# Performance work log

Hardware: AMD Instinct MI355X
Metric: run time of the kernel (lower is better)

The kernel has to match this reference:

```python
import jax, jax.numpy as jnp
import numpy as np

BINS = 200
DEPTH_MIN = 1.0
DEPTH_MAX = 80.0
ALPHA = 2.0
EPS = 1e-6
LOSS_WEIGHT = 1.0  # module attribute set externally in the repo; default 1.0
DMIN_LOG = float(np.log10(DEPTH_MIN))
INTERVAL = float((np.log10(DEPTH_MAX) - DMIN_LOG) / BINS)


def depth_to_bins_in_log(depth, mask):
    # truncation toward zero matches torch .to(torch.int)
    bins = ((jnp.log10(jnp.abs(depth)) - DMIN_LOG) / INTERVAL).astype(jnp.int32)
    bins = jnp.where(depth <= DEPTH_MIN, 0, bins)
    bins = jnp.where(depth >= DEPTH_MAX, BINS - 1, bins)
    bins = jnp.where(bins == BINS, BINS - 1, bins)
    bins = jnp.where(~mask, BINS + 1, bins)  # invalid pixels -> out-of-range id
    return bins


def setup_inputs() -> dict:
    key = jax.random.key(0)
    k1, k2, k3 = jax.random.split(key, 3)
    B, H, W = 4, 256, 384
    target = jax.random.uniform(k1, (B, 1, H, W), dtype=jnp.float32) * 100.0
    mask = jax.random.uniform(k2, (B, 1, H, W)) > 0.1
    pred_logit = jax.random.normal(k3, (B, BINS, H, W), dtype=jnp.float32)
    idx = jnp.arange(BINS, dtype=jnp.float32)
    # bins_weight[j, i] = exp(-alpha * (i - j)^2)
    bins_weight = jnp.exp(-ALPHA * (idx[None, :] - idx[:, None]) ** 2).astype(jnp.float32)
    return {"target": target, "mask": mask, "pred_logit": pred_logit, "bins_weight": bins_weight}


def reference(target, mask, pred_logit, bins_weight):
    B, C = pred_logit.shape[0], pred_logit.shape[1]
    gt_bins = depth_to_bins_in_log(target, mask)                 # [B,1,H,W] int32
    log_pred = jax.nn.log_softmax(pred_logit, axis=1)            # [B,C,H,W]
    log_pred = log_pred.reshape(B, C, -1).transpose(0, 2, 1)      # [B,N,C]
    gt_flat = gt_bins.reshape(B, -1)                              # [B,N]
    valid = gt_flat < C                                           # invalid rows -> zero weight
    # one_hot @ bins_weight is exactly a row-gather from bins_weight (zero row if invalid)
    weight = jnp.where(valid[..., None],
                       bins_weight[jnp.clip(gt_flat, 0, C - 1)],
                       jnp.zeros((), log_pred.dtype))             # [B,N,C]
    loss_pixels = -jnp.sum(weight * log_pred, axis=2)             # [B,N]
    valid_pixels = jnp.sum(mask).astype(log_pred.dtype)
    loss = jnp.sum(loss_pixels) / (valid_pixels + EPS)
    return loss * LOSS_WEIGHT
```

## Files before the change

kernel.cpp:

```cpp
#include <hip/hip_runtime.h>
#include <math.h>

#define C_BINS 200
#define PX 4

typedef float fv4 __attribute__((ext_vector_type(4)));
typedef int   iv4 __attribute__((ext_vector_type(4)));

__global__ __launch_bounds__(128) void dce_main_kernel(
    const float* __restrict__ target,
    const int*   __restrict__ mask,
    const float* __restrict__ logit,
    float*       __restrict__ ws,
    int HW)
{
    const int t  = blockIdx.x * blockDim.x + threadIdx.x;
    const int p0 = t * PX;
    const int b  = p0 / HW;
    const int hw = p0 - b * HW;

    const fv4 dep4 = *reinterpret_cast<const fv4*>(target + p0);
    const iv4 mk4  = *reinterpret_cast<const iv4*>(mask + p0);

    float gf[PX], valid[PX];
    #pragma unroll
    for (int j = 0; j < PX; ++j) {
        const float dj = dep4[j];
        int g;
        if (dj <= 1.0f) {
            g = 0;
        } else if (dj >= 80.0f) {
            g = 199;
        } else {
            g = (int)(log10f(dj) / 0.0095154499349597175f);
            g = (g > 199) ? 199 : g;
            g = (g < 0) ? 0 : g;
        }
        gf[j]    = (float)g;
        valid[j] = mk4[j] ? 1.0f : 0.0f;
    }

    const float* base = logit + (size_t)b * C_BINS * HW + hw;

    float m[PX], s[PX], dot[PX], sw[PX];
    #pragma unroll
    for (int j = 0; j < PX; ++j) { m[j] = -INFINITY; s[j] = 0.0f; dot[j] = 0.0f; sw[j] = 0.0f; }

    #pragma unroll 4
    for (int c = 0; c < C_BINS; ++c) {
        const fv4 x4 = __builtin_nontemporal_load(
            reinterpret_cast<const fv4*>(base + (size_t)c * HW));
        const float cf = (float)c;
        #pragma unroll
        for (int j = 0; j < PX; ++j) {
            const float x = x4[j];
            const float nm = fmaxf(m[j], x);
            const float e  = __expf(fminf(m[j], x) - nm);
            const bool  xg = x > m[j];
            s[j] = fmaf(s[j], xg ? e : 1.0f, xg ? 1.0f : e);
            m[j] = nm;
            const float d = cf - gf[j];
            const float w = __expf(-2.0f * d * d);
            dot[j] = fmaf(w, x, dot[j]);
            sw[j] += w;
        }
    }

    float lossp = 0.0f, vsum = 0.0f;
    #pragma unroll
    for (int j = 0; j < PX; ++j) {
        const float lse = m[j] + logf(s[j]);
        lossp += valid[j] * fmaf(lse, sw[j], -dot[j]);
        vsum  += valid[j];
    }

    #pragma unroll
    for (int off = 32; off > 0; off >>= 1) {
        lossp += __shfl_down(lossp, off);
        vsum  += __shfl_down(vsum, off);
    }
    __shared__ float sl[2], sv[2];
    const int wid = threadIdx.x >> 6;
    if ((threadIdx.x & 63) == 0) { sl[wid] = lossp; sv[wid] = vsum; }
    __syncthreads();
    if (threadIdx.x == 0) {
        atomicAdd(&ws[0], sl[0] + sl[1]);
        atomicAdd(&ws[1], sv[0] + sv[1]);
    }
}

__global__ void dce_final_kernel(const float* __restrict__ ws, float* __restrict__ out)
{
    out[0] = ws[0] / (ws[1] + 1e-6f);
}

extern "C" void kernel_launch(void* const* d_in, const int* in_sizes, int n_in,
                              void* d_out, int out_size, void* d_ws, size_t ws_size,
                              hipStream_t stream)
{
    const float* target = (const float*)d_in[0];
    const int*   mask   = (const int*)d_in[1];
    const float* logit  = (const float*)d_in[2];

    float* ws  = (float*)d_ws;
    float* out = (float*)d_out;

    const int npix = in_sizes[0];
    const int HW   = 256 * 384;

    (void)hipMemsetAsync(ws, 0, 2 * sizeof(float), stream);
    const int threads = 128;
    const int blocks  = npix / (threads * PX);
    dce_main_kernel<<<blocks, threads, 0, stream>>>(target, mask, logit, ws, HW);
    dce_final_kernel<<<1, 1, 0, stream>>>(ws, out);
}
```

Measured before the change: 478.7 us.

## Split channel loop across four wavefronts and merge online-softmax partials in LDS

Each block now covers 256 pixels using four wavefronts, and each wavefront processes a quarter of the 200 channels (50 each) instead of one thread looping over all channels. The partial max, sum-exp, weighted dot and weight sum are written to shared memory and merged by the first wavefront, which then does the loss reduction and atomics. This gives four times as many threads and shorter per-thread dependency chains, which should raise memory-level parallelism on a bandwidth-bound stream. The cost is an LDS merge step, a block barrier, and three idle wavefronts during the final reduction.

```diff
diff --git a/kernel.cpp b/kernel.cpp
--- a/kernel.cpp
+++ b/kernel.cpp
@@ -3,26 +3,30 @@
 
 #define C_BINS 200
 #define PX 4
+#define NW 4
+#define CPW 50
 
 typedef float fv4 __attribute__((ext_vector_type(4)));
 typedef int   iv4 __attribute__((ext_vector_type(4)));
 
-__global__ __launch_bounds__(128) void dce_main_kernel(
+__global__ __launch_bounds__(256) void dce_main_kernel(
     const float* __restrict__ target,
     const int*   __restrict__ mask,
     const float* __restrict__ logit,
     float*       __restrict__ ws,
     int HW)
 {
-    const int t  = blockIdx.x * blockDim.x + threadIdx.x;
-    const int p0 = t * PX;
-    const int b  = p0 / HW;
-    const int hw = p0 - b * HW;
+    const int lane = threadIdx.x & 63;
+    const int wv   = threadIdx.x >> 6;
+    const int pq   = blockIdx.x * 64 + lane;
+    const int p0   = pq * PX;
+    const int b    = p0 / HW;
+    const int hw   = p0 - b * HW;
 
     const fv4 dep4 = *reinterpret_cast<const fv4*>(target + p0);
     const iv4 mk4  = *reinterpret_cast<const iv4*>(mask + p0);
 
-    float gf[PX], valid[PX];
+    float gf[PX];
     #pragma unroll
     for (int j = 0; j < PX; ++j) {
         const float dj = dep4[j];
@@ -36,8 +40,7 @@
             g = (g > 199) ? 199 : g;
             g = (g < 0) ? 0 : g;
         }
-        gf[j]    = (float)g;
-        valid[j] = mk4[j] ? 1.0f : 0.0f;
+        gf[j] = (float)g;
     }
 
     const float* base = logit + (size_t)b * C_BINS * HW + hw;
@@ -46,8 +49,10 @@
     #pragma unroll
     for (int j = 0; j < PX; ++j) { m[j] = -INFINITY; s[j] = 0.0f; dot[j] = 0.0f; sw[j] = 0.0f; }
 
-    #pragma unroll 4
-    for (int c = 0; c < C_BINS; ++c) {
+    const int c0 = wv * CPW;
+    #pragma unroll 2
+    for (int ci = 0; ci < CPW; ++ci) {
+        const int c = c0 + ci;
         const fv4 x4 = __builtin_nontemporal_load(
             reinterpret_cast<const fv4*>(base + (size_t)c * HW));
         const float cf = (float)c;
@@ -66,26 +71,44 @@
         }
     }
 
-    float lossp = 0.0f, vsum = 0.0f;
+    __shared__ float lds[NW][64][PX][4];
     #pragma unroll
     for (int j = 0; j < PX; ++j) {
-        const float lse = m[j] + logf(s[j]);
-        lossp += valid[j] * fmaf(lse, sw[j], -dot[j]);
-        vsum  += valid[j];
+        lds[wv][lane][j][0] = m[j];
+        lds[wv][lane][j][1] = s[j];
+        lds[wv][lane][j][2] = dot[j];
+        lds[wv][lane][j][3] = sw[j];
     }
+    __syncthreads();
 
-    #pragma unroll
-    for (int off = 32; off > 0; off >>= 1) {
-        lossp += __shfl_down(lossp, off);
-        vsum  += __shfl_down(vsum, off);
-    }
-    __shared__ float sl[2], sv[2];
-    const int wid = threadIdx.x >> 6;
-    if ((threadIdx.x & 63) == 0) { sl[wid] = lossp; sv[wid] = vsum; }
-    __syncthreads();
-    if (threadIdx.x == 0) {
-        atomicAdd(&ws[0], sl[0] + sl[1]);
-        atomicAdd(&ws[1], sv[0] + sv[1]);
+    if (wv == 0) {
+        float lossp = 0.0f, vsum = 0.0f;
+        #pragma unroll
+        for (int j = 0; j < PX; ++j) {
+            float M = lds[0][lane][j][0];
+            #pragma unroll
+            for (int k = 1; k < NW; ++k) M = fmaxf(M, lds[k][lane][j][0]);
+            float S = 0.0f, D = 0.0f, W = 0.0f;
+            #pragma unroll
+            for (int k = 0; k < NW; ++k) {
+                S += lds[k][lane][j][1] * __expf(lds[k][lane][j][0] - M);
+                D += lds[k][lane][j][2];
+                W += lds[k][lane][j][3];
+            }
+            const float lse = M + logf(S);
+            const float v   = mk4[j] ? 1.0f : 0.0f;
+            lossp += v * fmaf(lse, W, -D);
+            vsum  += v;
+        }
+        #pragma unroll
+        for (int off = 32; off > 0; off >>= 1) {
+            lossp += __shfl_down(lossp, off);
+            vsum  += __shfl_down(vsum, off);
+        }
+        if (lane == 0) {
+            atomicAdd(&ws[0], lossp);
+            atomicAdd(&ws[1], vsum);
+        }
     }
 }
 
@@ -109,8 +132,8 @@
     const int HW   = 256 * 384;
 
     (void)hipMemsetAsync(ws, 0, 2 * sizeof(float), stream);
-    const int threads = 128;
-    const int blocks  = npix / (threads * PX);
+    const int threads = 256;
+    const int blocks  = npix / (64 * PX);
     dce_main_kernel<<<blocks, threads, 0, stream>>>(target, mask, logit, ws, HW);
     dce_final_kernel<<<1, 1, 0, stream>>>(ws, out);
 }
```

After: 416.9 us. -12.9%, faster.
